# Kernel optimization log

Hardware: AMD Instinct MI355X
Metric: run time of the kernel (lower is better)

The kernel has to match this reference:

```python
import jax, jax.numpy as jnp
import numpy as np


def setup_inputs() -> dict:
    key = jax.random.key(0)
    k1, k2, k3 = jax.random.split(key, 3)
    N = 524288
    T, C, R = 32, 7, 512
    texcoord = jax.random.uniform(k1, (N, 2), dtype=jnp.float32, minval=-1.0, maxval=1.0)
    mix_weights = jax.random.normal(k2, (N, T), dtype=jnp.float32)
    textures = jax.random.normal(k3, (T, C, R, R), dtype=jnp.float32)
    return {"texcoord": texcoord, "mix_weights": mix_weights, "textures": textures}


def _mixed_bilinear(texcoord, mix_weights, textures):
    # Faithful to F.grid_sample(mode='bilinear', padding_mode='zeros', align_corners=False)
    # followed by the mix-weight reduction over the texture dim, fused per corner.
    T, C, H, W = textures.shape
    in_shape = texcoord.shape
    tc = texcoord.reshape(-1, 2)           # [N, 2], (x, y) with x indexing W
    mw = mix_weights.reshape(-1, T)        # [N, T]

    x, y = tc[:, 0], tc[:, 1]
    # unnormalize (align_corners=False): pixel = ((coord + 1) * size - 1) / 2
    ix = ((x + 1.0) * W - 1.0) * 0.5
    iy = ((y + 1.0) * H - 1.0) * 0.5
    x0 = jnp.floor(ix)
    y0 = jnp.floor(iy)
    x1 = x0 + 1.0
    y1 = y0 + 1.0

    out = jnp.zeros((tc.shape[0], C), dtype=textures.dtype)
    corners = [
        (x0, y0, (x1 - ix) * (y1 - iy)),
        (x1, y0, (ix - x0) * (y1 - iy)),
        (x0, y1, (x1 - ix) * (iy - y0)),
        (x1, y1, (ix - x0) * (iy - y0)),
    ]
    for cx, cy, cw in corners:
        valid = (cx >= 0) & (cx <= W - 1) & (cy >= 0) & (cy <= H - 1)  # zeros padding
        xi = jnp.clip(cx, 0, W - 1).astype(jnp.int32)
        yi = jnp.clip(cy, 0, H - 1).astype(jnp.int32)
        g = textures[:, :, yi, xi]                      # [T, C, N] gather
        w = jnp.where(valid, cw, 0.0)                    # [N]
        out = out + jnp.einsum('n,nt,tcn->nc', w, mw, g)
    return out.reshape(in_shape[:-1] + (C,))


def reference(texcoord, mix_weights, textures):
    return _mixed_bilinear(texcoord, mix_weights, textures)
```

## Files before the change

### kernel.cpp

```cpp
#include <hip/hip_runtime.h>
#include <hip/hip_fp16.h>


#define RR 512
#define TT 32
#define CC 7
#define NBK 4096
#define NCH 256
#define CPP 2048
#define CHUNKS_PER_C 324
#define CSTRIDE 325

typedef float fx2 __attribute__((ext_vector_type(2)));
typedef float fx4 __attribute__((ext_vector_type(4)));
typedef _Float16 h2 __attribute__((ext_vector_type(2)));

__device__ __forceinline__ int bucket_of(float x, float y) {
    float ix = ((x + 1.0f) * 512.0f - 1.0f) * 0.5f;
    float iy = ((y + 1.0f) * 512.0f - 1.0f) * 0.5f;
    int xi0 = (int)fminf(fmaxf(floorf(ix), 0.0f), 511.0f);
    int yi0 = (int)fminf(fmaxf(floorf(iy), 0.0f), 511.0f);
    return ((yi0 >> 3) << 6) | (xi0 >> 3);
}

__global__ __launch_bounds__(256) void hist_pts(const fx2* __restrict__ tc2,
                                                int* __restrict__ cnt, int N) {
    __shared__ int h[NBK];
    int tid = threadIdx.x, ch = blockIdx.x;
    for (int q = tid; q < NBK; q += 256) h[q] = 0;
    __syncthreads();
    int base_n = ch * CPP;
#pragma unroll
    for (int i = 0; i < CPP / 256; ++i) {
        int n = base_n + i * 256 + tid;
        if (n < N) {
            fx2 xy = tc2[n];
            atomicAdd(&h[bucket_of(xy.x, xy.y)], 1);
        }
    }
    __syncthreads();
    for (int q = tid; q < NBK; q += 256) cnt[ch * NBK + q] = h[q];
}

__global__ __launch_bounds__(256) void col_prefix(int* __restrict__ cnt,
                                                  int* __restrict__ tot) {
    int b = blockIdx.x * 256 + threadIdx.x;
    int s = 0;
    for (int ch = 0; ch < NCH; ++ch) {
        int v = cnt[ch * NBK + b];
        cnt[ch * NBK + b] = s;
        s += v;
    }
    tot[b] = s;
}

__global__ __launch_bounds__(256) void scan_base(const int* __restrict__ tot,
                                                 int* __restrict__ base) {
    __shared__ int buf[NBK];
    __shared__ int part[256];
    int tid = threadIdx.x;
#pragma unroll
    for (int i = 0; i < 16; ++i) buf[tid * 16 + i] = tot[tid * 16 + i];
    int s = 0;
#pragma unroll
    for (int i = 0; i < 16; ++i) s += buf[tid * 16 + i];
    part[tid] = s;
    __syncthreads();
    for (int d = 1; d < 256; d <<= 1) {
        int v = (tid >= d) ? part[tid - d] : 0;
        __syncthreads();
        part[tid] += v;
        __syncthreads();
    }
    int run = part[tid] - s;
#pragma unroll
    for (int i = 0; i < 16; ++i) {
        base[tid * 16 + i] = run;
        run += buf[tid * 16 + i];
    }
    if (tid == 255) base[NBK] = run;
}

__global__ __launch_bounds__(256) void place_pts(const fx2* __restrict__ tc2,
                                                 const int* __restrict__ cnt,
                                                 const int* __restrict__ base,
                                                 fx4* __restrict__ recs, int N) {
    __shared__ int cur[NBK];
    int tid = threadIdx.x, ch = blockIdx.x;
    for (int q = tid; q < NBK; q += 256)
        cur[q] = base[q] + cnt[ch * NBK + q];
    __syncthreads();
    int base_n = ch * CPP;
#pragma unroll
    for (int i = 0; i < CPP / 256; ++i) {
        int n = base_n + i * 256 + tid;
        if (n < N) {
            fx2 xy = tc2[n];
            int slot = atomicAdd(&cur[bucket_of(xy.x, xy.y)], 1);
            fx4 rec = {xy.x, xy.y, __int_as_float(n), 0.0f};
            recs[slot] = rec;
        }
    }
}

__global__ __launch_bounds__(256) void transpose_tex_h(const float* __restrict__ src,
                                                       __half2* __restrict__ dst2) {
    __shared__ float tile[32][33];
    int b   = blockIdx.x;
    int xb  = (b & 15) << 5;
    int y   = (b >> 4) & 511;
    int c   = b >> 13;
    int tid = threadIdx.x;
    int xl  = tid & 31;
    int tq  = tid >> 5;
#pragma unroll
    for (int p = 0; p < 4; ++p) {
        int t = tq + p * 8;
        tile[t][xl] = src[((t * 7 + c) * 512 + y) * 512 + xb + xl];
    }
    __syncthreads();
#pragma unroll
    for (int p = 0; p < 2; ++p) {
        int o  = tid + p * 256;
        int x2 = o >> 4;
        int th = o & 15;
        dst2[((c * 512 + y) * 512 + xb + x2) * 16 + th] =
            __floats2half2_rn(tile[2 * th][x2], tile[2 * th + 1][x2]);
    }
}

__device__ __forceinline__ float dot_pos(const uint4* __restrict__ T, int idx,
                                         const h2* __restrict__ mh) {
    float d = 0.0f;
#pragma unroll
    for (int q = 0; q < 4; ++q) {
        union { uint4 u; h2 h[4]; } U;
        U.u = T[idx + q];
#pragma unroll
        for (int j = 0; j < 4; ++j) {
#if __has_builtin(__builtin_amdgcn_fdot2)
            d = __builtin_amdgcn_fdot2(U.h[j], mh[q * 4 + j], d, false);
#else
            d += (float)U.h[j].x * (float)mh[q * 4 + j].x
               + (float)U.h[j].y * (float)mh[q * 4 + j].y;
#endif
        }
    }
    return d;
}

__global__ __launch_bounds__(256) void mix_tile(const fx4* __restrict__ recs,
                                                const int* __restrict__ base,
                                                const fx4* __restrict__ mw4,
                                                const uint4* __restrict__ t16,
                                                float* __restrict__ out) {
    __shared__ uint4 TILE[7 * CSTRIDE];
    int k  = blockIdx.x;
    int tx = k & 63, ty = k >> 6;
    int X0 = tx << 3, Y0 = ty << 3;
    int tid = threadIdx.x;

    for (int q = tid; q < 7 * CHUNKS_PER_C; q += 256) {
        int c  = q / CHUNKS_PER_C;
        int r  = q - c * CHUNKS_PER_C;
        int yy = r / 36;
        int rr = r - yy * 36;
        int gx = X0 + (rr >> 2); if (gx > 511) gx = 511;
        int gy = Y0 + yy;        if (gy > 511) gy = 511;
        TILE[q + c] = t16[(size_t)((((c << 9) + gy) << 9) | gx) * 4 + (rr & 3)];
    }
    __syncthreads();

    int rbase = base[k];
    int cnt   = base[k + 1] - rbase;

    int sub = tid & 7;
    int c   = (sub == 7) ? 0 : sub;
    int cbase = c * CSTRIDE;

    int s = tid >> 3;
    if (s >= cnt) return;

    fx4 rec = recs[rbase + s];
    int n = __float_as_int(rec.z);
    fx4 m[8];
#pragma unroll
    for (int j = 0; j < 8; ++j) m[j] = mw4[(size_t)n * 8 + j];

    while (true) {
        int s2 = s + 32;
        bool live2 = s2 < cnt;
        fx4 rec2 = rec;
        if (live2) rec2 = recs[rbase + s2];

        float ix = ((rec.x + 1.0f) * 512.0f - 1.0f) * 0.5f;
        float iy = ((rec.y + 1.0f) * 512.0f - 1.0f) * 0.5f;
        float x0f = floorf(ix), y0f = floorf(iy);
        float fxw = ix - x0f, fyw = iy - y0f;
        float gxw = 1.0f - fxw, gyw = 1.0f - fyw;
        float w00 = gxw * gyw, w10 = fxw * gyw, w01 = gxw * fyw, w11 = fxw * fyw;
        bool vx0 = (x0f >= 0.0f), vx1 = (x0f <= 510.0f);
        bool vy0 = (y0f >= 0.0f), vy1 = (y0f <= 510.0f);
        if (!(vx0 && vy0)) w00 = 0.0f;
        if (!(vx1 && vy0)) w10 = 0.0f;
        if (!(vx0 && vy1)) w01 = 0.0f;
        if (!(vx1 && vy1)) w11 = 0.0f;
        int xi0 = (int)fminf(fmaxf(x0f, 0.0f), 511.0f);
        int xi1 = (int)fminf(fmaxf(x0f + 1.0f, 0.0f), 511.0f);
        int yi0 = (int)fminf(fmaxf(y0f, 0.0f), 511.0f);
        int yi1 = (int)fminf(fmaxf(y0f + 1.0f, 0.0f), 511.0f);
        int xl0 = xi0 - X0, xl1 = xi1 - X0;
        int yl0 = yi0 - Y0, yl1 = yi1 - Y0;

        h2 mh[16];
#pragma unroll
        for (int j = 0; j < 8; ++j) {
            mh[2 * j]     = h2{(_Float16)m[j].x, (_Float16)m[j].y};
            mh[2 * j + 1] = h2{(_Float16)m[j].z, (_Float16)m[j].w};
        }

        int p00 = cbase + ((yl0 * 9 + xl0) << 2);
        int p10 = cbase + ((yl0 * 9 + xl1) << 2);
        int p01 = cbase + ((yl1 * 9 + xl0) << 2);
        int p11 = cbase + ((yl1 * 9 + xl1) << 2);
        float d = w00 * dot_pos(TILE, p00, mh)
                + w10 * dot_pos(TILE, p10, mh)
                + w01 * dot_pos(TILE, p01, mh)
                + w11 * dot_pos(TILE, p11, mh);

        int nst = n;
        int n2 = 0;
        if (live2) {
            n2 = __float_as_int(rec2.z);
#pragma unroll
            for (int j = 0; j < 8; ++j) m[j] = mw4[(size_t)n2 * 8 + j];
        }

        if (sub < 7) __builtin_nontemporal_store(d, &out[(size_t)nst * 7 + c]);

        if (!live2) break;
        rec = rec2; n = n2; s = s2;
    }
}

__global__ __launch_bounds__(256) void mix_naive(const float* __restrict__ tc,
                                                 const float* __restrict__ mw,
                                                 const float* __restrict__ tex,
                                                 float* __restrict__ out, int N) {
    int n = blockIdx.x * 256 + threadIdx.x;
    if (n >= N) return;
    float x = tc[2 * n], y = tc[2 * n + 1];
    float ix = ((x + 1.0f) * 512.0f - 1.0f) * 0.5f;
    float iy = ((y + 1.0f) * 512.0f - 1.0f) * 0.5f;
    float x0f = floorf(ix), y0f = floorf(iy);
    float fx = ix - x0f, fy = iy - y0f;
    float gx = 1.0f - fx, gy = 1.0f - fy;
    float wgt[4] = {gx * gy, fx * gy, gx * fy, fx * fy};
    bool vx0 = (x0f >= 0.0f), vx1 = (x0f <= 510.0f);
    bool vy0 = (y0f >= 0.0f), vy1 = (y0f <= 510.0f);
    if (!(vx0 && vy0)) wgt[0] = 0.0f;
    if (!(vx1 && vy0)) wgt[1] = 0.0f;
    if (!(vx0 && vy1)) wgt[2] = 0.0f;
    if (!(vx1 && vy1)) wgt[3] = 0.0f;
    int xi0 = (int)fminf(fmaxf(x0f, 0.0f), 511.0f);
    int xi1 = (int)fminf(fmaxf(x0f + 1.0f, 0.0f), 511.0f);
    int yi0 = (int)fminf(fmaxf(y0f, 0.0f), 511.0f);
    int yi1 = (int)fminf(fmaxf(y0f + 1.0f, 0.0f), 511.0f);
    int xs[4] = {xi0, xi1, xi0, xi1};
    int ys[4] = {yi0, yi0, yi1, yi1};

    float acc[7] = {0.f, 0.f, 0.f, 0.f, 0.f, 0.f, 0.f};
#pragma unroll
    for (int kk = 0; kk < 4; ++kk) {
        float wk = wgt[kk];
        int base = ys[kk] * 512 + xs[kk];
        for (int t = 0; t < 32; ++t) {
            float m = wk * mw[(size_t)n * 32 + t];
#pragma unroll
            for (int cc = 0; cc < 7; ++cc)
                acc[cc] = fmaf(m, tex[(t * 7 + cc) * 262144 + base], acc[cc]);
        }
    }
#pragma unroll
    for (int cc = 0; cc < 7; ++cc) out[(size_t)n * 7 + cc] = acc[cc];
}

extern "C" void kernel_launch(void* const* d_in, const int* in_sizes, int n_in,
                              void* d_out, int out_size, void* d_ws, size_t ws_size,
                              hipStream_t stream) {
    const float* tc  = (const float*)d_in[0];
    const float* mw  = (const float*)d_in[1];
    const float* tex = (const float*)d_in[2];
    float* out = (float*)d_out;
    int N = in_sizes[0] / 2;

    const size_t TEXB = (size_t)CC * RR * RR * TT * sizeof(__half);
    const size_t RECB = (size_t)N * sizeof(fx4);
    const size_t CNTB = (size_t)NCH * NBK * sizeof(int);
    const size_t TOTB = (size_t)NBK * sizeof(int);
    const size_t BASB = (size_t)(NBK + 64) * sizeof(int);
    const size_t need = TEXB + RECB + CNTB + TOTB + BASB;

    if (ws_size >= need) {
        char* ws = (char*)d_ws;
        __half2* wst = (__half2*)ws;
        fx4* recs = (fx4*)(ws + TEXB);
        int* cnt  = (int*)(ws + TEXB + RECB);
        int* tot  = (int*)(ws + TEXB + RECB + CNTB);
        int* base = (int*)(ws + TEXB + RECB + CNTB + TOTB);

        hist_pts<<<NCH, 256, 0, stream>>>((const fx2*)tc, cnt, N);
        col_prefix<<<NBK / 256, 256, 0, stream>>>(cnt, tot);
        scan_base<<<1, 256, 0, stream>>>(tot, base);
        place_pts<<<NCH, 256, 0, stream>>>((const fx2*)tc, cnt, base, recs, N);
        transpose_tex_h<<<7 * 512 * 16, 256, 0, stream>>>(tex, wst);
        mix_tile<<<NBK, 256, 0, stream>>>((const fx4*)recs, (const int*)base,
                                          (const fx4*)mw, (const uint4*)wst, out);
    } else {
        mix_naive<<<(N + 255) / 256, 256, 0, stream>>>(tc, mw, tex, out, N);
    }
}
```

Baseline: 180.7 us.

## Fuse bucket-sort passes into one cooperative kernel with grid syncs

Replaces the four sort kernels (histogram, column prefix, base scan, placement) with one cooperative-launch kernel that separates the phases with grid-wide syncs. The column prefix is parallelised across 16 lanes per bucket using a shuffle scan instead of one serial thread per bucket walking 256 chunks. Point indexing changes from contiguous per-block chunks to a grid-strided loop. This removes three launch gaps and the serial column scan, at the cost of grid-sync overhead and a single block doing the base scan while the rest of the grid waits.

Measured after the change: 277.1 us. +53.4%, slower.

```diff
diff --git a/kernel.cpp b/kernel.cpp
--- a/kernel.cpp
+++ b/kernel.cpp
@@ -1,5 +1,8 @@
 #include <hip/hip_runtime.h>
 #include <hip/hip_fp16.h>
+#include <hip/hip_cooperative_groups.h>
+
+namespace cg = cooperative_groups;
 
 
 #define RR 512
@@ -7,7 +10,7 @@
 #define CC 7
 #define NBK 4096
 #define NCH 256
-#define CPP 2048
+#define GSTRIDE (NCH * 256)
 #define CHUNKS_PER_C 324
 #define CSTRIDE 325
 
@@ -23,83 +26,85 @@
     return ((yi0 >> 3) << 6) | (xi0 >> 3);
 }
 
-__global__ __launch_bounds__(256) void hist_pts(const fx2* __restrict__ tc2,
-                                                int* __restrict__ cnt, int N) {
+__global__ __launch_bounds__(256) void coop_sort(const fx2* __restrict__ tc2,
+                                                 int* __restrict__ cnt,
+                                                 int* __restrict__ tot,
+                                                 int* __restrict__ base,
+                                                 fx4* __restrict__ recs, int N) {
+    cg::grid_group grid = cg::this_grid();
     __shared__ int h[NBK];
+    __shared__ int part[256];
     int tid = threadIdx.x, ch = blockIdx.x;
+    int gt = ch * 256 + tid;
+
     for (int q = tid; q < NBK; q += 256) h[q] = 0;
     __syncthreads();
-    int base_n = ch * CPP;
-#pragma unroll
-    for (int i = 0; i < CPP / 256; ++i) {
-        int n = base_n + i * 256 + tid;
-        if (n < N) {
-            fx2 xy = tc2[n];
-            atomicAdd(&h[bucket_of(xy.x, xy.y)], 1);
-        }
+    for (int n = gt; n < N; n += GSTRIDE) {
+        fx2 xy = tc2[n];
+        atomicAdd(&h[bucket_of(xy.x, xy.y)], 1);
     }
     __syncthreads();
     for (int q = tid; q < NBK; q += 256) cnt[ch * NBK + q] = h[q];
-}
-
-__global__ __launch_bounds__(256) void col_prefix(int* __restrict__ cnt,
-                                                  int* __restrict__ tot) {
-    int b = blockIdx.x * 256 + threadIdx.x;
-    int s = 0;
-    for (int ch = 0; ch < NCH; ++ch) {
-        int v = cnt[ch * NBK + b];
-        cnt[ch * NBK + b] = s;
-        s += v;
-    }
-    tot[b] = s;
-}
-
-__global__ __launch_bounds__(256) void scan_base(const int* __restrict__ tot,
-                                                 int* __restrict__ base) {
-    __shared__ int buf[NBK];
-    __shared__ int part[256];
-    int tid = threadIdx.x;
-#pragma unroll
-    for (int i = 0; i < 16; ++i) buf[tid * 16 + i] = tot[tid * 16 + i];
-    int s = 0;
-#pragma unroll
-    for (int i = 0; i < 16; ++i) s += buf[tid * 16 + i];
-    part[tid] = s;
-    __syncthreads();
-    for (int d = 1; d < 256; d <<= 1) {
-        int v = (tid >= d) ? part[tid - d] : 0;
+    grid.sync();
+
+    {
+        int b  = gt >> 4;
+        int sl = gt & 15;
+        int vals[16];
+        int s = 0;
+#pragma unroll
+        for (int j = 0; j < 16; ++j) {
+            vals[j] = cnt[(sl * 16 + j) * NBK + b];
+            s += vals[j];
+        }
+        int incl = s;
+#pragma unroll
+        for (int d = 1; d < 16; d <<= 1) {
+            int t = __shfl_up(incl, d, 16);
+            if (sl >= d) incl += t;
+        }
+        int run = incl - s;
+#pragma unroll
+        for (int j = 0; j < 16; ++j) {
+            cnt[(sl * 16 + j) * NBK + b] = run;
+            run += vals[j];
+        }
+        if (sl == 15) tot[b] = run;
+    }
+    grid.sync();
+
+    if (ch == 0) {
+#pragma unroll
+        for (int i = 0; i < 16; ++i) h[tid * 16 + i] = tot[tid * 16 + i];
+        int s = 0;
+#pragma unroll
+        for (int i = 0; i < 16; ++i) s += h[tid * 16 + i];
+        part[tid] = s;
         __syncthreads();
-        part[tid] += v;
-        __syncthreads();
-    }
-    int run = part[tid] - s;
-#pragma unroll
-    for (int i = 0; i < 16; ++i) {
-        base[tid * 16 + i] = run;
-        run += buf[tid * 16 + i];
-    }
-    if (tid == 255) base[NBK] = run;
-}
-
-__global__ __launch_bounds__(256) void place_pts(const fx2* __restrict__ tc2,
-                                                 const int* __restrict__ cnt,
-                                                 const int* __restrict__ base,
-                                                 fx4* __restrict__ recs, int N) {
-    __shared__ int cur[NBK];
-    int tid = threadIdx.x, ch = blockIdx.x;
+        for (int d = 1; d < 256; d <<= 1) {
+            int v = (tid >= d) ? part[tid - d] : 0;
+            __syncthreads();
+            part[tid] += v;
+            __syncthreads();
+        }
+        int run = part[tid] - s;
+#pragma unroll
+        for (int i = 0; i < 16; ++i) {
+            base[tid * 16 + i] = run;
+            run += h[tid * 16 + i];
+        }
+        if (tid == 255) base[NBK] = run;
+    }
+    grid.sync();
+
     for (int q = tid; q < NBK; q += 256)
-        cur[q] = base[q] + cnt[ch * NBK + q];
-    __syncthreads();
-    int base_n = ch * CPP;
-#pragma unroll
-    for (int i = 0; i < CPP / 256; ++i) {
-        int n = base_n + i * 256 + tid;
-        if (n < N) {
-            fx2 xy = tc2[n];
-            int slot = atomicAdd(&cur[bucket_of(xy.x, xy.y)], 1);
-            fx4 rec = {xy.x, xy.y, __int_as_float(n), 0.0f};
-            recs[slot] = rec;
-        }
+        h[q] = base[q] + cnt[ch * NBK + q];
+    __syncthreads();
+    for (int n = gt; n < N; n += GSTRIDE) {
+        fx2 xy = tc2[n];
+        int slot = atomicAdd(&h[bucket_of(xy.x, xy.y)], 1);
+        fx4 rec = {xy.x, xy.y, __int_as_float(n), 0.0f};
+        recs[slot] = rec;
     }
 }
 
@@ -309,10 +314,11 @@
         int* tot  = (int*)(ws + TEXB + RECB + CNTB);
         int* base = (int*)(ws + TEXB + RECB + CNTB + TOTB);
 
-        hist_pts<<<NCH, 256, 0, stream>>>((const fx2*)tc, cnt, N);
-        col_prefix<<<NBK / 256, 256, 0, stream>>>(cnt, tot);
-        scan_base<<<1, 256, 0, stream>>>(tot, base);
-        place_pts<<<NCH, 256, 0, stream>>>((const fx2*)tc, cnt, base, recs, N);
+        const fx2* tc2 = (const fx2*)tc;
+        void* args[] = {(void*)&tc2, (void*)&cnt, (void*)&tot,
+                        (void*)&base, (void*)&recs, (void*)&N};
+        hipLaunchCooperativeKernel((const void*)coop_sort, dim3(NCH), dim3(256),
+                                   args, 0, stream);
         transpose_tex_h<<<7 * 512 * 16, 256, 0, stream>>>(tex, wst);
         mix_tile<<<NBK, 256, 0, stream>>>((const fx4*)recs, (const int*)base,
                                           (const fx4*)mw, (const uint4*)wst, out);
```
